# Kernel optimization log

Measured on AMD Instinct MI355X. Metric: run time of the kernel, lower is better.

## Reference

```python
import jax, jax.numpy as jnp
import numpy as np

N = 100000
E = 500000
HID = 256
N_EDGE_TYPES = 5
N_ATOM = 16
N_CHARGE = 7
NUM_RBF = 16
CUTOFF = 5.0
LN_EPS = 1e-5


def _xavier(key, shape):
    fan_in, fan_out = shape[0], shape[1]
    lim = float(np.sqrt(6.0 / (fan_in + fan_out)))
    return jax.random.uniform(key, shape, jnp.float32, -lim, lim)


def setup_inputs() -> dict:
    key = jax.random.key(0)
    ks = jax.random.split(key, 12)
    input_dim = HID * 2 + NUM_RBF + N_ATOM + N_CHARGE  # 551
    h = jax.random.normal(ks[0], (N, HID), jnp.float32)
    x = jax.random.normal(ks[1], (N, 3), jnp.float32)
    spawn_node_idx = jax.random.randint(ks[2], (E,), 0, N)
    existing_node_idx = jax.random.randint(ks[3], (E,), 0, N)
    ins_x = jax.random.normal(ks[4], (E, 3), jnp.float32)
    ins_a = jax.random.randint(ks[5], (E,), 0, N_ATOM)
    ins_c = jax.random.randint(ks[6], (E,), 0, N_CHARGE)
    # MLP params (Xavier weights, zero biases; LayerNorm gamma=1, beta=0)
    W1 = _xavier(ks[7], (input_dim, HID)); b1 = jnp.zeros((HID,), jnp.float32)
    g1 = jnp.ones((HID,), jnp.float32); be1 = jnp.zeros((HID,), jnp.float32)
    W2 = _xavier(ks[8], (HID, HID // 2)); b2 = jnp.zeros((HID // 2,), jnp.float32)
    g2 = jnp.ones((HID // 2,), jnp.float32); be2 = jnp.zeros((HID // 2,), jnp.float32)
    W3 = _xavier(ks[9], (HID // 2, N_EDGE_TYPES)); b3 = jnp.zeros((N_EDGE_TYPES,), jnp.float32)
    # Gaussian RBF parameters: centers on [0, cutoff], shared width from spacing
    rbf_mu = jnp.linspace(0.0, CUTOFF, NUM_RBF).astype(jnp.float32)
    delta = CUTOFF / (NUM_RBF - 1)
    rbf_gamma = jnp.asarray(1.0 / (2.0 * delta * delta), jnp.float32)
    return {"h": h, "x": x, "spawn_node_idx": spawn_node_idx,
            "existing_node_idx": existing_node_idx, "ins_x": ins_x,
            "ins_a": ins_a, "ins_c": ins_c,
            "W1": W1, "b1": b1, "g1": g1, "be1": be1,
            "W2": W2, "b2": b2, "g2": g2, "be2": be2,
            "W3": W3, "b3": b3, "rbf_mu": rbf_mu, "rbf_gamma": rbf_gamma}


def _layer_norm(z, gamma, beta):
    mu = jnp.mean(z, axis=-1, keepdims=True)
    var = jnp.mean((z - mu) ** 2, axis=-1, keepdims=True)
    return (z - mu) * jax.lax.rsqrt(var + LN_EPS) * gamma + beta


def reference(h, x, spawn_node_idx, existing_node_idx, ins_x, ins_a, ins_c,
              W1, b1, g1, be1, W2, b2, g2, be2, W3, b3, rbf_mu, rbf_gamma):
    # gather node pairs  [E, HID] / [E, 3]
    h_spawn = h[spawn_node_idx]
    h_existing = h[existing_node_idx]
    existing_pos = x[existing_node_idx]
    # distance + Gaussian RBF  [E, NUM_RBF]
    d = jnp.maximum(jnp.linalg.norm(ins_x - existing_pos, axis=-1), 1e-6)
    dist_features = jnp.exp(-rbf_gamma * (d[:, None] - rbf_mu) ** 2)
    # one-hot insertion type features
    ins_atom = jax.nn.one_hot(ins_a, N_ATOM, dtype=h.dtype)
    ins_charge = jax.nn.one_hot(ins_c, N_CHARGE, dtype=h.dtype)
    feats = jnp.concatenate([h_spawn, h_existing, dist_features, ins_atom, ins_charge], axis=-1)
    # 3-layer MLP: Linear -> LN -> SiLU -> Linear -> LN -> SiLU -> Linear
    z = jax.nn.silu(_layer_norm(feats @ W1 + b1, g1, be1))
    z = jax.nn.silu(_layer_norm(z @ W2 + b2, g2, be2))
    return z @ W3 + b3  # [E, N_EDGE_TYPES]
```

## Files before the change

### kernel.cpp

```cpp
#include <hip/hip_runtime.h>
#include <stdint.h>

#define NN 100000
#define EE 500000
#define HIDD 256
#define LN_EPS 1e-5f

typedef _Float16 half8 __attribute__((ext_vector_type(8)));
typedef _Float16 half4 __attribute__((ext_vector_type(4)));
typedef __fp16 fp16x2 __attribute__((ext_vector_type(2)));
typedef float f32x4 __attribute__((ext_vector_type(4)));
typedef float f32x2 __attribute__((ext_vector_type(2)));

#define LBAR() asm volatile("s_waitcnt lgkmcnt(0)\n\ts_barrier" ::: "memory")

__device__ __forceinline__ unsigned short f2h(float f) {
  _Float16 h = (_Float16)f;
  union { _Float16 hh; unsigned short us; } u; u.hh = h;
  return u.us;
}

__device__ __forceinline__ unsigned pkrtz(float a, float b) {
  union { fp16x2 h; unsigned u; } c;
  c.h = __builtin_amdgcn_cvt_pkrtz(a, b);
  return c.u;
}

__device__ __forceinline__ float fast_silu(float y) {
  float e = __expf(-y);
  return y * __builtin_amdgcn_rcpf(1.f + e);
}

__device__ __forceinline__ half8 ldg8(const unsigned short* p) {
  return *(const half8*)p;
}

__device__ __forceinline__ int4 cvt_row(const float* s) {
  float4 a0 = *(const float4*)s, a1 = *(const float4*)(s + 4);
  uint4 ua;
  ua.x = pkrtz(a0.x, a0.y); ua.y = pkrtz(a0.z, a0.w);
  ua.z = pkrtz(a1.x, a1.y); ua.w = pkrtz(a1.z, a1.w);
  return *(int4*)&ua;
}


__global__ __launch_bounds__(256) void prep_w(const float* __restrict__ W1,
                                              const float* __restrict__ W2,
                                              const float* __restrict__ W3,
                                              unsigned short* __restrict__ wc,
                                              unsigned short* __restrict__ w1f,
                                              unsigned short* __restrict__ w2sw,
                                              unsigned short* __restrict__ w3sw) {
  int t = blockIdx.x * 256 + threadIdx.x;
  if (t < 131072) {
    int kq = t >> 12, mm = (t >> 3) & 511, j = t & 7;
    int k = kq * 8 + j;
    int row = k + ((mm < 256) ? 0 : 256);
    wc[t] = f2h(W1[row * 256 + (mm & 255)]);
  } else if (t < 147456) {
    int t2 = t - 131072;
    int kq = t2 >> 11, m = (t2 >> 3) & 255, j = t2 & 7;
    int k = 512 + kq * 8 + j;
    w1f[t2] = f2h((k < 551) ? W1[k * 256 + m] : 0.f);
  } else if (t < 180224) {
    int t2 = t - 147456;
    int chunk = t2 >> 13, rem = t2 & 8191;
    int kq = rem >> 10, n = (rem >> 3) & 127, j = rem & 7;
    int k = (chunk << 6) + (kq << 3) + j;
    w2sw[t2] = f2h(W2[k * 128 + n]);
  } else if (t < 182272) {
    int t3 = t - 180224;
    int kq = t3 >> 7, o = (t3 >> 3) & 15, j = t3 & 7;
    int k = (kq << 3) + j;
    w3sw[t3] = f2h((o < 5) ? W3[k * 5 + o] : 0.f);
  }
}

__global__ __launch_bounds__(256) void pgemm(const float* __restrict__ h,
                                             const unsigned short* __restrict__ wc,
                                             unsigned short* __restrict__ Pb) {
  __shared__ short hl[16384];
  const int bid = blockIdx.x;
  const int tile = bid >> 1, ch = bid & 1;
  const int nb = tile * 64;
  const int t = threadIdx.x;
  const int lane = t & 63;
  const int wv = t >> 6;
  const int cl = lane & 15;
  const int q = lane >> 4;
  const int sx = (cl & 7) << 3;

  const int row0 = t >> 3, p0 = t & 7;
  const int row1 = row0 + 32;
  const int n0 = (nb + row0 < NN) ? nb + row0 : NN - 1;
  const int n1 = (nb + row1 < NN) ? nb + row1 : NN - 1;
  const int sw0e = (row0 & 7) << 3;
  const int sw1e = (row1 & 7) << 3;
#pragma unroll
  for (int c = 0; c < 4; ++c) {
    int4 v0 = cvt_row(h + (size_t)n0 * 256 + c * 64 + p0 * 8);
    int4 v1 = cvt_row(h + (size_t)n1 * 256 + c * 64 + p0 * 8);
    *(int4*)&hl[row0 * 256 + ((c * 64 + p0 * 8) ^ sw0e)] = v0;
    *(int4*)&hl[row1 * 256 + ((c * 64 + p0 * 8) ^ sw1e)] = v1;
  }
  LBAR();

  const unsigned short* wcp = wc + q * 4096 + (size_t)(ch * 256 + wv * 64 + cl) * 8;
  f32x4 acc[4][4];
#pragma unroll
  for (int i = 0; i < 4; ++i)
#pragma unroll
    for (int j = 0; j < 4; ++j) acc[i][j] = (f32x4){0.f, 0.f, 0.f, 0.f};

#pragma unroll
  for (int c = 0; c < 4; ++c)
#pragma unroll
    for (int ks = 0; ks < 2; ++ks) {
      half8 bf[4], fX[4];
#pragma unroll
      for (int j = 0; j < 4; ++j)
        bf[j] = *(const half8*)&hl[(j * 16 + cl) * 256 + ((c * 64 + ks * 32 + q * 8) ^ sx)];
#pragma unroll
      for (int i = 0; i < 4; ++i) fX[i] = ldg8(wcp + (c * 2 + ks) * 16384 + i * 128);
#pragma unroll
      for (int i = 0; i < 4; ++i)
#pragma unroll
        for (int j = 0; j < 4; ++j)
          acc[i][j] = __builtin_amdgcn_mfma_f32_16x16x32_f16(fX[i], bf[j], acc[i][j], 0, 0, 0);
    }

#pragma unroll
  for (int i = 0; i < 4; ++i)
#pragma unroll
    for (int j = 0; j < 4; ++j) {
      int n = nb + cl + 16 * j;
      if (n < NN) {
        int mm = ch * 256 + wv * 64 + i * 16 + q * 4;
        uint2 w;
        w.x = pkrtz(acc[i][j][0], acc[i][j][1]);
        w.y = pkrtz(acc[i][j][2], acc[i][j][3]);
        *(uint2*)(Pb + (size_t)n * 512 + mm) = w;
      }
    }
}

struct __align__(16) SMemN {
  short r1[16384];
  short feats[4096];
  float red[512];
  _Float16 b1h[256], g1h[256], be1h[256];
  _Float16 b2h[128], g2h[128], be2h[128];
  float muv[16];
  float b3v[8];
  int spI[64], exI[64];
};

__global__ __launch_bounds__(256, 3)
void edge_head_main(const float* __restrict__ x,
                    const int* __restrict__ spawn, const int* __restrict__ exist,
                    const float* __restrict__ insx, const int* __restrict__ insa,
                    const int* __restrict__ insc,
                    const float* __restrict__ b1, const float* __restrict__ g1,
                    const float* __restrict__ be1,
                    const float* __restrict__ b2, const float* __restrict__ g2,
                    const float* __restrict__ be2,
                    const float* __restrict__ b3, const float* __restrict__ mu,
                    const float* __restrict__ gammaP,
                    const unsigned short* __restrict__ w1f,
                    const unsigned short* __restrict__ w2sw,
                    const unsigned short* __restrict__ w3swg,
                    const unsigned short* __restrict__ Pb,
                    float* __restrict__ out) {
  __shared__ SMemN sm;
  const int t = threadIdx.x;
  const int base = blockIdx.x * 64;
  const int lane = t & 63;
  const int wv = t >> 6;
  const int cl = lane & 15;
  const int q = lane >> 4;
  const int sx = (cl & 7) << 3;

  sm.b1h[t] = (_Float16)b1[t]; sm.g1h[t] = (_Float16)g1[t]; sm.be1h[t] = (_Float16)be1[t];
  if (t < 128) { sm.b2h[t] = (_Float16)b2[t]; sm.g2h[t] = (_Float16)g2[t]; sm.be2h[t] = (_Float16)be2[t]; }
  if (t < 16) sm.muv[t] = mu[t];
  if (t < 8) sm.b3v[t] = (t < 5) ? b3[t] : 0.f;
  if (t < 64) {
    int e = base + t; int ec = e < EE ? e : EE - 1;
    sm.spI[t] = spawn[ec]; sm.exI[t] = exist[ec];
  }
  const float gma = gammaP[0];

  LBAR();

  const unsigned short* pb1[4];
  const unsigned short* pb2[4];
#pragma unroll
  for (int j = 0; j < 4; ++j) {
    int n = cl + 16 * j;
    pb1[j] = Pb + (size_t)sm.spI[n] * 512 + wv * 64 + q * 4;
    pb2[j] = Pb + (size_t)sm.exI[n] * 512 + 256 + wv * 64 + q * 4;
  }
  half4 p1v[4][4], p2v[4][4];
#pragma unroll
  for (int i = 0; i < 4; ++i)
#pragma unroll
    for (int j = 0; j < 4; ++j) p1v[i][j] = *(const half4*)(pb1[j] + i * 16);
#pragma unroll
  for (int i = 0; i < 4; ++i)
#pragma unroll
    for (int j = 0; j < 4; ++j) p2v[i][j] = *(const half4*)(pb2[j] + i * 16);

  if (t < 64) {
    int e = base + t; int ec = e < EE ? e : EE - 1;
    float ix0 = insx[ec * 3], ix1 = insx[ec * 3 + 1], ix2 = insx[ec * 3 + 2];
    int nd = sm.exI[t];
    float dx = ix0 - x[nd * 3], dy = ix1 - x[nd * 3 + 1], dz = ix2 - x[nd * 3 + 2];
    float d = fmaxf(sqrtf(dx * dx + dy * dy + dz * dz), 1e-6f);
    int k1 = 16 + insa[ec], k2 = 32 + insc[ec];
    short* rp = &sm.feats[t * 64];
    const int sw = t & 7;
    float rb[16];
#pragma unroll
    for (int k = 0; k < 16; ++k) { float dd = d - sm.muv[k]; rb[k] = __expf(-gma * dd * dd); }
    uint4 ua, ub;
    ua.x = pkrtz(rb[0], rb[1]);  ua.y = pkrtz(rb[2], rb[3]);
    ua.z = pkrtz(rb[4], rb[5]);  ua.w = pkrtz(rb[6], rb[7]);
    ub.x = pkrtz(rb[8], rb[9]);  ub.y = pkrtz(rb[10], rb[11]);
    ub.z = pkrtz(rb[12], rb[13]); ub.w = pkrtz(rb[14], rb[15]);
    *(int4*)&rp[(0 ^ sw) * 8] = *(int4*)&ua;
    *(int4*)&rp[(1 ^ sw) * 8] = *(int4*)&ub;
    const int4 z4 = {0, 0, 0, 0};
#pragma unroll
    for (int g = 2; g < 8; ++g) *(int4*)&rp[(g ^ sw) * 8] = z4;
    rp[((k1 >> 3) ^ sw) * 8 + (k1 & 7)] = (short)0x3C00;
    rp[((k2 >> 3) ^ sw) * 8 + (k2 & 7)] = (short)0x3C00;
  }

  LBAR();

  f32x4 acc[4][4];
#pragma unroll
  for (int i = 0; i < 4; ++i)
#pragma unroll
    for (int j = 0; j < 4; ++j) {
      f32x4 a;
      a[0] = (float)p1v[i][j][0] + (float)p2v[i][j][0];
      a[1] = (float)p1v[i][j][1] + (float)p2v[i][j][1];
      a[2] = (float)p1v[i][j][2] + (float)p2v[i][j][2];
      a[3] = (float)p1v[i][j][3] + (float)p2v[i][j][3];
      acc[i][j] = a;
    }
  {
    const unsigned short* w1fp = w1f + q * 2048 + wv * 512 + cl * 8;
#pragma unroll
    for (int ks = 0; ks < 2; ++ks) {
      half8 bf[4], fX[4];
#pragma unroll
      for (int j = 0; j < 4; ++j)
        bf[j] = *(const half8*)&sm.feats[(j * 16 + cl) * 64 + ((ks * 32 + q * 8) ^ sx)];
#pragma unroll
      for (int i = 0; i < 4; ++i) fX[i] = ldg8(w1fp + ks * 8192 + i * 128);
#pragma unroll
      for (int i = 0; i < 4; ++i)
#pragma unroll
        for (int j = 0; j < 4; ++j)
          acc[i][j] = __builtin_amdgcn_mfma_f32_16x16x32_f16(fX[i], bf[j], acc[i][j], 0, 0, 0);
    }
  }

  f32x2 bb1[4][2];
#pragma unroll
  for (int i = 0; i < 4; ++i) {
    half4 b4 = *(const half4*)&sm.b1h[wv * 64 + i * 16 + q * 4];
    bb1[i][0] = (f32x2){(float)b4[0], (float)b4[1]};
    bb1[i][1] = (f32x2){(float)b4[2], (float)b4[3]};
  }
  float S1arr[4], Q1arr[4];
#pragma unroll
  for (int j = 0; j < 4; ++j) {
    f32x2 S2 = (f32x2){0.f, 0.f}, Q2 = (f32x2){0.f, 0.f};
#pragma unroll
    for (int i = 0; i < 4; ++i) {
      f32x2 v0 = (f32x2){acc[i][j][0], acc[i][j][1]} + bb1[i][0];
      f32x2 v1 = (f32x2){acc[i][j][2], acc[i][j][3]} + bb1[i][1];
      acc[i][j][0] = v0[0]; acc[i][j][1] = v0[1];
      acc[i][j][2] = v1[0]; acc[i][j][3] = v1[1];
      S2 += v0 + v1;
      Q2 += v0 * v0;
      Q2 += v1 * v1;
    }
    float S = S2[0] + S2[1], Q = Q2[0] + Q2[1];
    S += __shfl_xor(S, 16); S += __shfl_xor(S, 32);
    Q += __shfl_xor(Q, 16); Q += __shfl_xor(Q, 32);
    S1arr[j] = S; Q1arr[j] = Q;
  }
  if (q == 0) {
#pragma unroll
    for (int j = 0; j < 4; ++j) {
      sm.red[wv * 64 + j * 16 + cl] = S1arr[j];
      sm.red[256 + wv * 64 + j * 16 + cl] = Q1arr[j];
    }
  }
  LBAR();
  f32x2 rs1[4], mr1[4];
#pragma unroll
  for (int j = 0; j < 4; ++j) {
    int m = j * 16 + cl;
    float S = sm.red[m] + sm.red[64 + m] + sm.red[128 + m] + sm.red[192 + m];
    float Q = sm.red[256 + m] + sm.red[320 + m] + sm.red[384 + m] + sm.red[448 + m];
    float mn = S * (1.f / 256.f);
    float rs = rsqrtf(Q * (1.f / 256.f) - mn * mn + LN_EPS);
    rs1[j] = (f32x2){rs, rs};
    mr1[j] = (f32x2){-mn * rs, -mn * rs};
  }
#pragma unroll
  for (int i = 0; i < 4; ++i) {
    half4 g4 = *(const half4*)&sm.g1h[wv * 64 + i * 16 + q * 4];
    half4 e4 = *(const half4*)&sm.be1h[wv * 64 + i * 16 + q * 4];
    f32x2 gg0 = (f32x2){(float)g4[0], (float)g4[1]}, gg1 = (f32x2){(float)g4[2], (float)g4[3]};
    f32x2 ee0 = (f32x2){(float)e4[0], (float)e4[1]}, ee1 = (f32x2){(float)e4[2], (float)e4[3]};
#pragma unroll
    for (int j = 0; j < 4; ++j) {
      f32x2 v0 = (f32x2){acc[i][j][0], acc[i][j][1]};
      f32x2 v1 = (f32x2){acc[i][j][2], acc[i][j][3]};
      f32x2 t0 = v0 * rs1[j] + mr1[j];
      f32x2 t1 = v1 * rs1[j] + mr1[j];
      f32x2 y0 = t0 * gg0 + ee0;
      f32x2 y1 = t1 * gg1 + ee1;
      float s0 = fast_silu(y0[0]), s1 = fast_silu(y0[1]);
      float s2 = fast_silu(y1[0]), s3 = fast_silu(y1[1]);
      uint2 w; w.x = pkrtz(s0, s1); w.y = pkrtz(s2, s3);
      int m = j * 16 + cl;
      int k0 = wv * 64 + i * 16 + q * 4;
      *(uint2*)&sm.r1[m * 256 + (k0 ^ ((m & 7) << 3))] = w;
    }
  }
  LBAR();

  half8 af3[4];
#pragma unroll
  for (int ks = 0; ks < 4; ++ks)
    af3[ks] = ldg8(w3swg + (ks * 4 + q) * 128 + cl * 8);

  const unsigned short* w2p = w2sw + q * 1024 + wv * 256 + cl * 8;
  f32x4 acc2[2][4];
#pragma unroll
  for (int i = 0; i < 2; ++i)
#pragma unroll
    for (int j = 0; j < 4; ++j) acc2[i][j] = (f32x4){0.f, 0.f, 0.f, 0.f};
#pragma unroll
  for (int c2 = 0; c2 < 4; ++c2) {
#pragma unroll
    for (int ks = 0; ks < 2; ++ks) {
      half8 a0 = ldg8(w2p + c2 * 8192 + ks * 4096);
      half8 a1 = ldg8(w2p + c2 * 8192 + ks * 4096 + 128);
      half8 bf[4];
#pragma unroll
      for (int j = 0; j < 4; ++j)
        bf[j] = *(const half8*)&sm.r1[(j * 16 + cl) * 256 + ((c2 * 64 + ks * 32 + q * 8) ^ sx)];
#pragma unroll
      for (int j = 0; j < 4; ++j) {
        acc2[0][j] = __builtin_amdgcn_mfma_f32_16x16x32_f16(a0, bf[j], acc2[0][j], 0, 0, 0);
        acc2[1][j] = __builtin_amdgcn_mfma_f32_16x16x32_f16(a1, bf[j], acc2[1][j], 0, 0, 0);
      }
    }
  }

  f32x2 bb2[2][2];
#pragma unroll
  for (int i = 0; i < 2; ++i) {
    half4 b4 = *(const half4*)&sm.b2h[wv * 32 + i * 16 + q * 4];
    bb2[i][0] = (f32x2){(float)b4[0], (float)b4[1]};
    bb2[i][1] = (f32x2){(float)b4[2], (float)b4[3]};
  }
  float S2arr[4], Q2arr[4];
#pragma unroll
  for (int j = 0; j < 4; ++j) {
    f32x2 S2 = (f32x2){0.f, 0.f}, Q2 = (f32x2){0.f, 0.f};
#pragma unroll
    for (int i = 0; i < 2; ++i) {
      f32x2 v0 = (f32x2){acc2[i][j][0], acc2[i][j][1]} + bb2[i][0];
      f32x2 v1 = (f32x2){acc2[i][j][2], acc2[i][j][3]} + bb2[i][1];
      acc2[i][j][0] = v0[0]; acc2[i][j][1] = v0[1];
      acc2[i][j][2] = v1[0]; acc2[i][j][3] = v1[1];
      S2 += v0 + v1;
      Q2 += v0 * v0;
      Q2 += v1 * v1;
    }
    float S = S2[0] + S2[1], Q = Q2[0] + Q2[1];
    S += __shfl_xor(S, 16); S += __shfl_xor(S, 32);
    Q += __shfl_xor(Q, 16); Q += __shfl_xor(Q, 32);
    S2arr[j] = S; Q2arr[j] = Q;
  }
  if (q == 0) {
#pragma unroll
    for (int j = 0; j < 4; ++j) {
      sm.red[wv * 64 + j * 16 + cl] = S2arr[j];
      sm.red[256 + wv * 64 + j * 16 + cl] = Q2arr[j];
    }
  }
  LBAR();
  f32x2 rs2[4], mr2[4];
#pragma unroll
  for (int j = 0; j < 4; ++j) {
    int m = j * 16 + cl;
    float S = sm.red[m] + sm.red[64 + m] + sm.red[128 + m] + sm.red[192 + m];
    float Q = sm.red[256 + m] + sm.red[320 + m] + sm.red[384 + m] + sm.red[448 + m];
    float mn = S * (1.f / 128.f);
    float rs = rsqrtf(Q * (1.f / 128.f) - mn * mn + LN_EPS);
    rs2[j] = (f32x2){rs, rs};
    mr2[j] = (f32x2){-mn * rs, -mn * rs};
  }
#pragma unroll
  for (int i = 0; i < 2; ++i) {
    half4 g4 = *(const half4*)&sm.g2h[wv * 32 + i * 16 + q * 4];
    half4 e4 = *(const half4*)&sm.be2h[wv * 32 + i * 16 + q * 4];
    f32x2 gg0 = (f32x2){(float)g4[0], (float)g4[1]}, gg1 = (f32x2){(float)g4[2], (float)g4[3]};
    f32x2 ee0 = (f32x2){(float)e4[0], (float)e4[1]}, ee1 = (f32x2){(float)e4[2], (float)e4[3]};
#pragma unroll
    for (int j = 0; j < 4; ++j) {
      f32x2 v0 = (f32x2){acc2[i][j][0], acc2[i][j][1]};
      f32x2 v1 = (f32x2){acc2[i][j][2], acc2[i][j][3]};
      f32x2 t0 = v0 * rs2[j] + mr2[j];
      f32x2 t1 = v1 * rs2[j] + mr2[j];
      f32x2 y0 = t0 * gg0 + ee0;
      f32x2 y1 = t1 * gg1 + ee1;
      float s0 = fast_silu(y0[0]), s1 = fast_silu(y0[1]);
      float s2 = fast_silu(y1[0]), s3 = fast_silu(y1[1]);
      uint2 w; w.x = pkrtz(s0, s1); w.y = pkrtz(s2, s3);
      int m = j * 16 + cl;
      int k0 = wv * 32 + i * 16 + q * 4;
      *(uint2*)&sm.r1[m * 128 + (k0 ^ ((m & 7) << 3))] = w;
    }
  }
  LBAR();

  f32x4 a3 = (f32x4){0.f, 0.f, 0.f, 0.f};
  const int m3 = wv * 16 + cl;
  const int sx3 = (m3 & 7) << 3;
#pragma unroll
  for (int ks = 0; ks < 4; ++ks) {
    half8 bfv = *(const half8*)&sm.r1[m3 * 128 + ((ks * 32 + q * 8) ^ sx3)];
    a3 = __builtin_amdgcn_mfma_f32_16x16x32_f16(af3[ks], bfv, a3, 0, 0, 0);
  }
#pragma unroll
  for (int r = 0; r < 4; ++r) {
    int o = q * 4 + r;
    if (o < 5) sm.red[m3 * 5 + o] = a3[r] + sm.b3v[o];
  }
  LBAR();
  if (t < 80) {
    size_t g = (size_t)base * 5 + (size_t)t * 4;
    if (g + 4 <= (size_t)EE * 5) {
      *(float4*)(out + g) = *(const float4*)&sm.red[t * 4];
    } else {
#pragma unroll
      for (int u = 0; u < 4; ++u)
        if (g + u < (size_t)EE * 5) out[g + u] = sm.red[t * 4 + u];
    }
  }
}


__global__ __launch_bounds__(256) void prep_fb(const float* __restrict__ W1,
                                               const float* __restrict__ W2,
                                               const float* __restrict__ W3,
                                               unsigned short* __restrict__ w1sw,
                                               unsigned short* __restrict__ w2sw,
                                               unsigned short* __restrict__ w3sw) {
  int t = blockIdx.x * 256 + threadIdx.x;
  if (t < 147456) {
    int chunk = t >> 14, rem = t & 16383;
    int kq = rem >> 11, n = (rem >> 3) & 255, j = rem & 7;
    int k = (chunk << 6) + (kq << 3) + j;
    w1sw[t] = f2h((k < 551) ? W1[k * 256 + n] : 0.f);
  } else if (t < 180224) {
    int t2 = t - 147456;
    int chunk = t2 >> 13, rem = t2 & 8191;
    int kq = rem >> 10, n = (rem >> 3) & 127, j = rem & 7;
    int k = (chunk << 6) + (kq << 3) + j;
    w2sw[t2] = f2h(W2[k * 128 + n]);
  } else if (t < 182272) {
    int t3 = t - 180224;
    int kq = t3 >> 7, o = (t3 >> 3) & 15, j = t3 & 7;
    int k = (kq << 3) + j;
    w3sw[t3] = f2h((o < 5) ? W3[k * 5 + o] : 0.f);
  }
}

struct __align__(16) SMemF {
  short r1[16384];
  short feats[4096];
  float red[512];
  _Float16 b1h[256], g1h[256], be1h[256];
  _Float16 b2h[128], g2h[128], be2h[128];
  float muv[16];
  float b3v[8];
  int spI[64], exI[64];
};

__global__ __launch_bounds__(256, 3)
void edge_head_fb(const float* __restrict__ h, const float* __restrict__ x,
                  const int* __restrict__ spawn, const int* __restrict__ exist,
                  const float* __restrict__ insx, const int* __restrict__ insa,
                  const int* __restrict__ insc,
                  const float* __restrict__ b1, const float* __restrict__ g1,
                  const float* __restrict__ be1,
                  const float* __restrict__ b2, const float* __restrict__ g2,
                  const float* __restrict__ be2,
                  const float* __restrict__ b3, const float* __restrict__ mu,
                  const float* __restrict__ gammaP,
                  const unsigned short* __restrict__ w1sw,
                  const unsigned short* __restrict__ w2sw,
                  const unsigned short* __restrict__ w3swg,
                  float* __restrict__ out) {
  __shared__ SMemF sm;
  const int t = threadIdx.x;
  const int base = blockIdx.x * 64;
  const int lane = t & 63;
  const int wv = t >> 6;
  const int cl = lane & 15;
  const int q = lane >> 4;
  const int sx = (cl & 7) << 3;

  sm.b1h[t] = (_Float16)b1[t]; sm.g1h[t] = (_Float16)g1[t]; sm.be1h[t] = (_Float16)be1[t];
  if (t < 128) { sm.b2h[t] = (_Float16)b2[t]; sm.g2h[t] = (_Float16)g2[t]; sm.be2h[t] = (_Float16)be2[t]; }
  if (t < 16) sm.muv[t] = mu[t];
  if (t < 8) sm.b3v[t] = (t < 5) ? b3[t] : 0.f;
  if (t < 64) {
    int e = base + t; int ec = e < EE ? e : EE - 1;
    sm.spI[t] = spawn[ec]; sm.exI[t] = exist[ec];
  }
  const float gma = gammaP[0];
  LBAR();

  float dreg = 0.f;
  int k1 = 16, k2 = 32;
  if (t < 64) {
    int e = base + t; int ec = e < EE ? e : EE - 1;
    float ix0 = insx[ec * 3], ix1 = insx[ec * 3 + 1], ix2 = insx[ec * 3 + 2];
    int nd = sm.exI[t];
    float dx = ix0 - x[nd * 3], dy = ix1 - x[nd * 3 + 1], dz = ix2 - x[nd * 3 + 2];
    dreg = fmaxf(sqrtf(dx * dx + dy * dy + dz * dz), 1e-6f);
    k1 = 16 + insa[ec]; k2 = 32 + insc[ec];
  }

  const int row0 = t >> 3, p0 = t & 7;
  const int row1 = row0 + 32;
  const int sw0 = ((p0 ^ (row0 & 7)) << 3);
  const int sw1 = ((p0 ^ (row1 & 7)) << 3);

  const float* bSp0 = h + (size_t)sm.spI[row0] * HIDD + p0 * 8;
  const float* bSp1 = h + (size_t)sm.spI[row1] * HIDD + p0 * 8;
  const float* bEx0 = h + (size_t)sm.exI[row0] * HIDD + p0 * 8;
  const float* bEx1 = h + (size_t)sm.exI[row1] * HIDD + p0 * 8;

  int4 pS0, pS1, pS2, pS3;
#define GLOAD2F(ph) do {                                                \
    const float* b0_ = ((ph) < 2) ? bSp0 : bEx0;                        \
    const float* b1_ = ((ph) < 2) ? bSp1 : bEx1;                        \
    const int ce_ = ((ph) & 1) * 128;                                   \
    pS0 = cvt_row(b0_ + ce_);                                           \
    pS1 = cvt_row(b1_ + ce_);                                           \
    pS2 = cvt_row(b0_ + ce_ + 64);                                      \
    pS3 = cvt_row(b1_ + ce_ + 64);                                      \
  } while (0)

  GLOAD2F(0);
  *(int4*)&sm.r1[row0 * 64 + sw0] = pS0;
  *(int4*)&sm.r1[row1 * 64 + sw1] = pS1;
  *(int4*)&sm.r1[4096 + row0 * 64 + sw0] = pS2;
  *(int4*)&sm.r1[4096 + row1 * 64 + sw1] = pS3;
  GLOAD2F(1);

  const unsigned short* w1p = w1sw + q * 2048 + wv * 512 + cl * 8;

  if (t < 64) {
    short* rp = &sm.feats[t * 64];
    const int sw = t & 7;
    float rb[16];
#pragma unroll
    for (int k = 0; k < 16; ++k) { float dd = dreg - sm.muv[k]; rb[k] = __expf(-gma * dd * dd); }
    uint4 ua, ub;
    ua.x = pkrtz(rb[0], rb[1]);  ua.y = pkrtz(rb[2], rb[3]);
    ua.z = pkrtz(rb[4], rb[5]);  ua.w = pkrtz(rb[6], rb[7]);
    ub.x = pkrtz(rb[8], rb[9]);  ub.y = pkrtz(rb[10], rb[11]);
    ub.z = pkrtz(rb[12], rb[13]); ub.w = pkrtz(rb[14], rb[15]);
    *(int4*)&rp[(0 ^ sw) * 8] = *(int4*)&ua;
    *(int4*)&rp[(1 ^ sw) * 8] = *(int4*)&ub;
    const int4 z4 = {0, 0, 0, 0};
#pragma unroll
    for (int g = 2; g < 8; ++g) *(int4*)&rp[(g ^ sw) * 8] = z4;
    rp[((k1 >> 3) ^ sw) * 8 + (k1 & 7)] = (short)0x3C00;
    rp[((k2 >> 3) ^ sw) * 8 + (k2 & 7)] = (short)0x3C00;
  }
  LBAR();

  f32x4 acc[4][4];
#pragma unroll
  for (int i = 0; i < 4; ++i)
#pragma unroll
    for (int j = 0; j < 4; ++j) acc[i][j] = (f32x4){0.f, 0.f, 0.f, 0.f};

#pragma unroll
  for (int p = 0; p < 4; ++p) {
    if (p < 3) {
      const int nb = ((p + 1) & 1) * 8192;
      *(int4*)&sm.r1[nb + row0 * 64 + sw0] = pS0;
      *(int4*)&sm.r1[nb + row1 * 64 + sw1] = pS1;
      *(int4*)&sm.r1[nb + 4096 + row0 * 64 + sw0] = pS2;
      *(int4*)&sm.r1[nb + 4096 + row1 * 64 + sw1] = pS3;
      if (p < 2) GLOAD2F(p + 2);
    }
    const int cb = (p & 1) * 8192;
#pragma unroll
    for (int ch = 0; ch < 2; ++ch) {
      const unsigned short* wp = w1p + (2 * p + ch) * 16384;
#pragma unroll
      for (int ks = 0; ks < 2; ++ks) {
        half8 bf[4], fX[4];
#pragma unroll
        for (int j = 0; j < 4; ++j)
          bf[j] = *(const half8*)&sm.r1[cb + ch * 4096 + (j * 16 + cl) * 64 + ((ks * 32 + q * 8) ^ sx)];
#pragma unroll
        for (int i = 0; i < 4; ++i) fX[i] = ldg8(wp + ks * 8192 + i * 128);
#pragma unroll
        for (int i = 0; i < 4; ++i)
#pragma unroll
          for (int j = 0; j < 4; ++j)
            acc[i][j] = __builtin_amdgcn_mfma_f32_16x16x32_f16(fX[i], bf[j], acc[i][j], 0, 0, 0);
      }
    }
    if (p < 3) LBAR();
  }
#undef GLOAD2F

  {
    const unsigned short* wp = w1p + 8 * 16384;
#pragma unroll
    for (int ks = 0; ks < 2; ++ks) {
      half8 bf[4], fX[4];
#pragma unroll
      for (int j = 0; j < 4; ++j)
        bf[j] = *(const half8*)&sm.feats[(j * 16 + cl) * 64 + ((ks * 32 + q * 8) ^ sx)];
#pragma unroll
      for (int i = 0; i < 4; ++i) fX[i] = ldg8(wp + ks * 8192 + i * 128);
#pragma unroll
      for (int i = 0; i < 4; ++i)
#pragma unroll
        for (int j = 0; j < 4; ++j)
          acc[i][j] = __builtin_amdgcn_mfma_f32_16x16x32_f16(fX[i], bf[j], acc[i][j], 0, 0, 0);
    }
  }

  f32x2 bb1[4][2];
#pragma unroll
  for (int i = 0; i < 4; ++i) {
    half4 b4 = *(const half4*)&sm.b1h[wv * 64 + i * 16 + q * 4];
    bb1[i][0] = (f32x2){(float)b4[0], (float)b4[1]};
    bb1[i][1] = (f32x2){(float)b4[2], (float)b4[3]};
  }
  float S1arr[4], Q1arr[4];
#pragma unroll
  for (int j = 0; j < 4; ++j) {
    f32x2 S2 = (f32x2){0.f, 0.f}, Q2 = (f32x2){0.f, 0.f};
#pragma unroll
    for (int i = 0; i < 4; ++i) {
      f32x2 v0 = (f32x2){acc[i][j][0], acc[i][j][1]} + bb1[i][0];
      f32x2 v1 = (f32x2){acc[i][j][2], acc[i][j][3]} + bb1[i][1];
      acc[i][j][0] = v0[0]; acc[i][j][1] = v0[1];
      acc[i][j][2] = v1[0]; acc[i][j][3] = v1[1];
      S2 += v0 + v1; Q2 += v0 * v0; Q2 += v1 * v1;
    }
    float S = S2[0] + S2[1], Q = Q2[0] + Q2[1];
    S += __shfl_xor(S, 16); S += __shfl_xor(S, 32);
    Q += __shfl_xor(Q, 16); Q += __shfl_xor(Q, 32);
    S1arr[j] = S; Q1arr[j] = Q;
  }
  if (q == 0) {
#pragma unroll
    for (int j = 0; j < 4; ++j) {
      sm.red[wv * 64 + j * 16 + cl] = S1arr[j];
      sm.red[256 + wv * 64 + j * 16 + cl] = Q1arr[j];
    }
  }
  LBAR();
  f32x2 rs1[4], mr1[4];
#pragma unroll
  for (int j = 0; j < 4; ++j) {
    int m = j * 16 + cl;
    float S = sm.red[m] + sm.red[64 + m] + sm.red[128 + m] + sm.red[192 + m];
    float Q = sm.red[256 + m] + sm.red[320 + m] + sm.red[384 + m] + sm.red[448 + m];
    float mn = S * (1.f / 256.f);
    float rs = rsqrtf(Q * (1.f / 256.f) - mn * mn + LN_EPS);
    rs1[j] = (f32x2){rs, rs};
    mr1[j] = (f32x2){-mn * rs, -mn * rs};
  }
#pragma unroll
  for (int i = 0; i < 4; ++i) {
    half4 g4 = *(const half4*)&sm.g1h[wv * 64 + i * 16 + q * 4];
    half4 e4 = *(const half4*)&sm.be1h[wv * 64 + i * 16 + q * 4];
    f32x2 gg0 = (f32x2){(float)g4[0], (float)g4[1]}, gg1 = (f32x2){(float)g4[2], (float)g4[3]};
    f32x2 ee0 = (f32x2){(float)e4[0], (float)e4[1]}, ee1 = (f32x2){(float)e4[2], (float)e4[3]};
#pragma unroll
    for (int j = 0; j < 4; ++j) {
      f32x2 v0 = (f32x2){acc[i][j][0], acc[i][j][1]};
      f32x2 v1 = (f32x2){acc[i][j][2], acc[i][j][3]};
      f32x2 t0 = v0 * rs1[j] + mr1[j];
      f32x2 t1 = v1 * rs1[j] + mr1[j];
      f32x2 y0 = t0 * gg0 + ee0;
      f32x2 y1 = t1 * gg1 + ee1;
      float s0 = fast_silu(y0[0]), s1 = fast_silu(y0[1]);
      float s2 = fast_silu(y1[0]), s3 = fast_silu(y1[1]);
      uint2 w; w.x = pkrtz(s0, s1); w.y = pkrtz(s2, s3);
      int m = j * 16 + cl;
      int k0 = wv * 64 + i * 16 + q * 4;
      *(uint2*)&sm.r1[m * 256 + (k0 ^ ((m & 7) << 3))] = w;
    }
  }
  LBAR();

  half8 af3[4];
#pragma unroll
  for (int ks = 0; ks < 4; ++ks)
    af3[ks] = ldg8(w3swg + (ks * 4 + q) * 128 + cl * 8);

  const unsigned short* w2p = w2sw + q * 1024 + wv * 256 + cl * 8;
  f32x4 acc2[2][4];
#pragma unroll
  for (int i = 0; i < 2; ++i)
#pragma unroll
    for (int j = 0; j < 4; ++j) acc2[i][j] = (f32x4){0.f, 0.f, 0.f, 0.f};
#pragma unroll
  for (int c2 = 0; c2 < 4; ++c2) {
#pragma unroll
    for (int ks = 0; ks < 2; ++ks) {
      half8 a0 = ldg8(w2p + c2 * 8192 + ks * 4096);
      half8 a1 = ldg8(w2p + c2 * 8192 + ks * 4096 + 128);
      half8 bf[4];
#pragma unroll
      for (int j = 0; j < 4; ++j)
        bf[j] = *(const half8*)&sm.r1[(j * 16 + cl) * 256 + ((c2 * 64 + ks * 32 + q * 8) ^ sx)];
#pragma unroll
      for (int j = 0; j < 4; ++j) {
        acc2[0][j] = __builtin_amdgcn_mfma_f32_16x16x32_f16(a0, bf[j], acc2[0][j], 0, 0, 0);
        acc2[1][j] = __builtin_amdgcn_mfma_f32_16x16x32_f16(a1, bf[j], acc2[1][j], 0, 0, 0);
      }
    }
  }

  f32x2 bb2[2][2];
#pragma unroll
  for (int i = 0; i < 2; ++i) {
    half4 b4 = *(const half4*)&sm.b2h[wv * 32 + i * 16 + q * 4];
    bb2[i][0] = (f32x2){(float)b4[0], (float)b4[1]};
    bb2[i][1] = (f32x2){(float)b4[2], (float)b4[3]};
  }
  float S2arr[4], Q2arr[4];
#pragma unroll
  for (int j = 0; j < 4; ++j) {
    f32x2 S2 = (f32x2){0.f, 0.f}, Q2 = (f32x2){0.f, 0.f};
#pragma unroll
    for (int i = 0; i < 2; ++i) {
      f32x2 v0 = (f32x2){acc2[i][j][0], acc2[i][j][1]} + bb2[i][0];
      f32x2 v1 = (f32x2){acc2[i][j][2], acc2[i][j][3]} + bb2[i][1];
      acc2[i][j][0] = v0[0]; acc2[i][j][1] = v0[1];
      acc2[i][j][2] = v1[0]; acc2[i][j][3] = v1[1];
      S2 += v0 + v1; Q2 += v0 * v0; Q2 += v1 * v1;
    }
    float S = S2[0] + S2[1], Q = Q2[0] + Q2[1];
    S += __shfl_xor(S, 16); S += __shfl_xor(S, 32);
    Q += __shfl_xor(Q, 16); Q += __shfl_xor(Q, 32);
    S2arr[j] = S; Q2arr[j] = Q;
  }
  if (q == 0) {
#pragma unroll
    for (int j = 0; j < 4; ++j) {
      sm.red[wv * 64 + j * 16 + cl] = S2arr[j];
      sm.red[256 + wv * 64 + j * 16 + cl] = Q2arr[j];
    }
  }
  LBAR();
  f32x2 rs2[4], mr2[4];
#pragma unroll
  for (int j = 0; j < 4; ++j) {
    int m = j * 16 + cl;
    float S = sm.red[m] + sm.red[64 + m] + sm.red[128 + m] + sm.red[192 + m];
    float Q = sm.red[256 + m] + sm.red[320 + m] + sm.red[384 + m] + sm.red[448 + m];
    float mn = S * (1.f / 128.f);
    float rs = rsqrtf(Q * (1.f / 128.f) - mn * mn + LN_EPS);
    rs2[j] = (f32x2){rs, rs};
    mr2[j] = (f32x2){-mn * rs, -mn * rs};
  }
#pragma unroll
  for (int i = 0; i < 2; ++i) {
    half4 g4 = *(const half4*)&sm.g2h[wv * 32 + i * 16 + q * 4];
    half4 e4 = *(const half4*)&sm.be2h[wv * 32 + i * 16 + q * 4];
    f32x2 gg0 = (f32x2){(float)g4[0], (float)g4[1]}, gg1 = (f32x2){(float)g4[2], (float)g4[3]};
    f32x2 ee0 = (f32x2){(float)e4[0], (float)e4[1]}, ee1 = (f32x2){(float)e4[2], (float)e4[3]};
#pragma unroll
    for (int j = 0; j < 4; ++j) {
      f32x2 v0 = (f32x2){acc2[i][j][0], acc2[i][j][1]};
      f32x2 v1 = (f32x2){acc2[i][j][2], acc2[i][j][3]};
      f32x2 t0 = v0 * rs2[j] + mr2[j];
      f32x2 t1 = v1 * rs2[j] + mr2[j];
      f32x2 y0 = t0 * gg0 + ee0;
      f32x2 y1 = t1 * gg1 + ee1;
      float s0 = fast_silu(y0[0]), s1 = fast_silu(y0[1]);
      float s2 = fast_silu(y1[0]), s3 = fast_silu(y1[1]);
      uint2 w; w.x = pkrtz(s0, s1); w.y = pkrtz(s2, s3);
      int m = j * 16 + cl;
      int k0 = wv * 32 + i * 16 + q * 4;
      *(uint2*)&sm.r1[m * 128 + (k0 ^ ((m & 7) << 3))] = w;
    }
  }
  LBAR();

  f32x4 a3 = (f32x4){0.f, 0.f, 0.f, 0.f};
  const int m3 = wv * 16 + cl;
  const int sx3 = (m3 & 7) << 3;
#pragma unroll
  for (int ks = 0; ks < 4; ++ks) {
    half8 bfv = *(const half8*)&sm.r1[m3 * 128 + ((ks * 32 + q * 8) ^ sx3)];
    a3 = __builtin_amdgcn_mfma_f32_16x16x32_f16(af3[ks], bfv, a3, 0, 0, 0);
  }
#pragma unroll
  for (int r = 0; r < 4; ++r) {
    int o = q * 4 + r;
    if (o < 5) sm.red[m3 * 5 + o] = a3[r] + sm.b3v[o];
  }
  LBAR();
  if (t < 80) {
    size_t g = (size_t)base * 5 + (size_t)t * 4;
    if (g + 4 <= (size_t)EE * 5) {
      *(float4*)(out + g) = *(const float4*)&sm.red[t * 4];
    } else {
#pragma unroll
      for (int u = 0; u < 4; ++u)
        if (g + u < (size_t)EE * 5) out[g + u] = sm.red[t * 4 + u];
    }
  }
}

extern "C" void kernel_launch(void* const* d_in, const int* in_sizes, int n_in,
                              void* d_out, int out_size, void* d_ws, size_t ws_size,
                              hipStream_t stream) {
  const float* h    = (const float*)d_in[0];
  const float* x    = (const float*)d_in[1];
  const int* spawn  = (const int*)d_in[2];
  const int* exist  = (const int*)d_in[3];
  const float* insx = (const float*)d_in[4];
  const int* insa   = (const int*)d_in[5];
  const int* insc   = (const int*)d_in[6];
  const float* W1   = (const float*)d_in[7];
  const float* b1   = (const float*)d_in[8];
  const float* g1   = (const float*)d_in[9];
  const float* be1  = (const float*)d_in[10];
  const float* W2   = (const float*)d_in[11];
  const float* b2   = (const float*)d_in[12];
  const float* g2   = (const float*)d_in[13];
  const float* be2  = (const float*)d_in[14];
  const float* W3   = (const float*)d_in[15];
  const float* b3   = (const float*)d_in[16];
  const float* mu   = (const float*)d_in[17];
  const float* gma  = (const float*)d_in[18];

  const size_t needP = 364544ull + (size_t)NN * 512 * 2;
  if (ws_size >= needP) {
    unsigned short* wc   = (unsigned short*)d_ws;
    unsigned short* w1f  = wc + 131072;
    unsigned short* w2sw = w1f + 16384;
    unsigned short* w3sw = w2sw + 32768;
    unsigned short* Pb   = w3sw + 2048;
    prep_w<<<712, 256, 0, stream>>>(W1, W2, W3, wc, w1f, w2sw, w3sw);
    pgemm<<<3126, 256, 0, stream>>>(h, wc, Pb);
    edge_head_main<<<7813, 256, 0, stream>>>(x, spawn, exist, insx, insa, insc,
                                             b1, g1, be1, b2, g2, be2, b3, mu, gma,
                                             w1f, w2sw, w3sw, Pb, (float*)d_out);
  } else {
    unsigned short* w1sw = (unsigned short*)d_ws;
    unsigned short* w2sw = w1sw + 147456;
    unsigned short* w3sw = w2sw + 32768;
    prep_fb<<<712, 256, 0, stream>>>(W1, W2, W3, w1sw, w2sw, w3sw);
    edge_head_fb<<<7813, 256, 0, stream>>>(h, x, spawn, exist, insx, insa, insc,
                                           b1, g1, be1, b2, g2, be2, b3, mu, gma,
                                           w1sw, w2sw, w3sw, (float*)d_out);
  }
}
```

Measured before the change: 427.4 us.

## Merge pgemm column halves, fold bias into projection, raise edge kernel occupancy

New measurement: 434.8 us. Within noise of the previous version (+1.7%).

```diff
diff --git a/kernel.cpp b/kernel.cpp
--- a/kernel.cpp
+++ b/kernel.cpp
@@ -77,12 +77,11 @@
 }
 
 __global__ __launch_bounds__(256) void pgemm(const float* __restrict__ h,
+                                             const float* __restrict__ b1,
                                              const unsigned short* __restrict__ wc,
                                              unsigned short* __restrict__ Pb) {
   __shared__ short hl[16384];
-  const int bid = blockIdx.x;
-  const int tile = bid >> 1, ch = bid & 1;
-  const int nb = tile * 64;
+  const int nb = blockIdx.x * 64;
   const int t = threadIdx.x;
   const int lane = t & 63;
   const int wv = t >> 6;
@@ -105,63 +104,71 @@
   }
   LBAR();
 
-  const unsigned short* wcp = wc + q * 4096 + (size_t)(ch * 256 + wv * 64 + cl) * 8;
-  f32x4 acc[4][4];
-#pragma unroll
-  for (int i = 0; i < 4; ++i)
-#pragma unroll
-    for (int j = 0; j < 4; ++j) acc[i][j] = (f32x4){0.f, 0.f, 0.f, 0.f};
-
-#pragma unroll
-  for (int c = 0; c < 4; ++c)
-#pragma unroll
-    for (int ks = 0; ks < 2; ++ks) {
-      half8 bf[4], fX[4];
-#pragma unroll
-      for (int j = 0; j < 4; ++j)
-        bf[j] = *(const half8*)&hl[(j * 16 + cl) * 256 + ((c * 64 + ks * 32 + q * 8) ^ sx)];
-#pragma unroll
-      for (int i = 0; i < 4; ++i) fX[i] = ldg8(wcp + (c * 2 + ks) * 16384 + i * 128);
+#pragma unroll
+  for (int ch = 0; ch < 2; ++ch) {
+    const unsigned short* wcp = wc + q * 4096 + (size_t)(ch * 256 + wv * 64 + cl) * 8;
+    f32x4 acc[4][4];
+    if (ch == 0) {
+#pragma unroll
+      for (int i = 0; i < 4; ++i) {
+        float4 bv = *(const float4*)(b1 + wv * 64 + i * 16 + q * 4);
+#pragma unroll
+        for (int j = 0; j < 4; ++j) acc[i][j] = (f32x4){bv.x, bv.y, bv.z, bv.w};
+      }
+    } else {
 #pragma unroll
       for (int i = 0; i < 4; ++i)
 #pragma unroll
+        for (int j = 0; j < 4; ++j) acc[i][j] = (f32x4){0.f, 0.f, 0.f, 0.f};
+    }
+#pragma unroll
+    for (int c = 0; c < 4; ++c)
+#pragma unroll
+      for (int ks = 0; ks < 2; ++ks) {
+        half8 bf[4], fX[4];
+#pragma unroll
         for (int j = 0; j < 4; ++j)
-          acc[i][j] = __builtin_amdgcn_mfma_f32_16x16x32_f16(fX[i], bf[j], acc[i][j], 0, 0, 0);
-    }
-
-#pragma unroll
-  for (int i = 0; i < 4; ++i)
-#pragma unroll
-    for (int j = 0; j < 4; ++j) {
-      int n = nb + cl + 16 * j;
-      if (n < NN) {
-        int mm = ch * 256 + wv * 64 + i * 16 + q * 4;
-        uint2 w;
-        w.x = pkrtz(acc[i][j][0], acc[i][j][1]);
-        w.y = pkrtz(acc[i][j][2], acc[i][j][3]);
-        *(uint2*)(Pb + (size_t)n * 512 + mm) = w;
+          bf[j] = *(const half8*)&hl[(j * 16 + cl) * 256 + ((c * 64 + ks * 32 + q * 8) ^ sx)];
+#pragma unroll
+        for (int i = 0; i < 4; ++i) fX[i] = ldg8(wcp + (c * 2 + ks) * 16384 + i * 128);
+#pragma unroll
+        for (int i = 0; i < 4; ++i)
+#pragma unroll
+          for (int j = 0; j < 4; ++j)
+            acc[i][j] = __builtin_amdgcn_mfma_f32_16x16x32_f16(fX[i], bf[j], acc[i][j], 0, 0, 0);
       }
-    }
+#pragma unroll
+    for (int i = 0; i < 4; ++i)
+#pragma unroll
+      for (int j = 0; j < 4; ++j) {
+        int n = nb + cl + 16 * j;
+        if (n < NN) {
+          int mm = ch * 256 + wv * 64 + i * 16 + q * 4;
+          uint2 w;
+          w.x = pkrtz(acc[i][j][0], acc[i][j][1]);
+          w.y = pkrtz(acc[i][j][2], acc[i][j][3]);
+          *(uint2*)(Pb + (size_t)n * 512 + mm) = w;
+        }
+      }
+  }
 }
 
 struct __align__(16) SMemN {
   short r1[16384];
-  short feats[4096];
   float red[512];
-  _Float16 b1h[256], g1h[256], be1h[256];
+  _Float16 g1h[256], be1h[256];
   _Float16 b2h[128], g2h[128], be2h[128];
   float muv[16];
   float b3v[8];
   int spI[64], exI[64];
 };
 
-__global__ __launch_bounds__(256, 3)
+__global__ __launch_bounds__(256, 4)
 void edge_head_main(const float* __restrict__ x,
                     const int* __restrict__ spawn, const int* __restrict__ exist,
                     const float* __restrict__ insx, const int* __restrict__ insa,
                     const int* __restrict__ insc,
-                    const float* __restrict__ b1, const float* __restrict__ g1,
-                    const float* __restrict__ be1,
+                    const float* __restrict__ g1, const float* __restrict__ be1,
                     const float* __restrict__ b2, const float* __restrict__ g2,
                     const float* __restrict__ be2,
                     const float* __restrict__ b3, const float* __restrict__ mu,
@@ -180,7 +187,7 @@
   const int q = lane >> 4;
   const int sx = (cl & 7) << 3;
 
-  sm.b1h[t] = (_Float16)b1[t]; sm.g1h[t] = (_Float16)g1[t]; sm.be1h[t] = (_Float16)be1[t];
+  sm.g1h[t] = (_Float16)g1[t]; sm.be1h[t] = (_Float16)be1[t];
   if (t < 128) { sm.b2h[t] = (_Float16)b2[t]; sm.g2h[t] = (_Float16)g2[t]; sm.be2h[t] = (_Float16)be2[t]; }
   if (t < 16) sm.muv[t] = mu[t];
   if (t < 8) sm.b3v[t] = (t < 5) ? b3[t] : 0.f;
@@ -200,15 +207,15 @@
     pb1[j] = Pb + (size_t)sm.spI[n] * 512 + wv * 64 + q * 4;
     pb2[j] = Pb + (size_t)sm.exI[n] * 512 + 256 + wv * 64 + q * 4;
   }
-  half4 p1v[4][4], p2v[4][4];
-#pragma unroll
-  for (int i = 0; i < 4; ++i)
-#pragma unroll
-    for (int j = 0; j < 4; ++j) p1v[i][j] = *(const half4*)(pb1[j] + i * 16);
-#pragma unroll
-  for (int i = 0; i < 4; ++i)
-#pragma unroll
-    for (int j = 0; j < 4; ++j) p2v[i][j] = *(const half4*)(pb2[j] + i * 16);
+  half4 p1a[2][4], p2a[2][4];
+#pragma unroll
+  for (int i2 = 0; i2 < 2; ++i2)
+#pragma unroll
+    for (int j = 0; j < 4; ++j) p1a[i2][j] = *(const half4*)(pb1[j] + i2 * 16);
+#pragma unroll
+  for (int i2 = 0; i2 < 2; ++i2)
+#pragma unroll
+    for (int j = 0; j < 4; ++j) p2a[i2][j] = *(const half4*)(pb2[j] + i2 * 16);
 
   if (t < 64) {
     int e = base + t; int ec = e < EE ? e : EE - 1;
@@ -217,7 +224,7 @@
     float dx = ix0 - x[nd * 3], dy = ix1 - x[nd * 3 + 1], dz = ix2 - x[nd * 3 + 2];
     float d = fmaxf(sqrtf(dx * dx + dy * dy + dz * dz), 1e-6f);
     int k1 = 16 + insa[ec], k2 = 32 + insc[ec];
-    short* rp = &sm.feats[t * 64];
+    short* rp = &sm.r1[t * 64];
     const int sw = t & 7;
     float rb[16];
 #pragma unroll
@@ -236,19 +243,40 @@
     rp[((k2 >> 3) ^ sw) * 8 + (k2 & 7)] = (short)0x3C00;
   }
 
+  half4 p1b[2][4], p2b[2][4];
+#pragma unroll
+  for (int i2 = 0; i2 < 2; ++i2)
+#pragma unroll
+    for (int j = 0; j < 4; ++j) p1b[i2][j] = *(const half4*)(pb1[j] + (2 + i2) * 16);
+#pragma unroll
+  for (int i2 = 0; i2 < 2; ++i2)
+#pragma unroll
+    for (int j = 0; j < 4; ++j) p2b[i2][j] = *(const half4*)(pb2[j] + (2 + i2) * 16);
+
   LBAR();
 
   f32x4 acc[4][4];
 #pragma unroll
-  for (int i = 0; i < 4; ++i)
+  for (int i2 = 0; i2 < 2; ++i2)
 #pragma unroll
     for (int j = 0; j < 4; ++j) {
       f32x4 a;
-      a[0] = (float)p1v[i][j][0] + (float)p2v[i][j][0];
-      a[1] = (float)p1v[i][j][1] + (float)p2v[i][j][1];
-      a[2] = (float)p1v[i][j][2] + (float)p2v[i][j][2];
-      a[3] = (float)p1v[i][j][3] + (float)p2v[i][j][3];
-      acc[i][j] = a;
+      a[0] = (float)p1a[i2][j][0] + (float)p2a[i2][j][0];
+      a[1] = (float)p1a[i2][j][1] + (float)p2a[i2][j][1];
+      a[2] = (float)p1a[i2][j][2] + (float)p2a[i2][j][2];
+      a[3] = (float)p1a[i2][j][3] + (float)p2a[i2][j][3];
+      acc[i2][j] = a;
+    }
+#pragma unroll
+  for (int i2 = 0; i2 < 2; ++i2)
+#pragma unroll
+    for (int j = 0; j < 4; ++j) {
+      f32x4 a;
+      a[0] = (float)p1b[i2][j][0] + (float)p2b[i2][j][0];
+      a[1] = (float)p1b[i2][j][1] + (float)p2b[i2][j][1];
+      a[2] = (float)p1b[i2][j][2] + (float)p2b[i2][j][2];
+      a[3] = (float)p1b[i2][j][3] + (float)p2b[i2][j][3];
+      acc[2 + i2][j] = a;
     }
   {
     const unsigned short* w1fp = w1f + q * 2048 + wv * 512 + cl * 8;
@@ -257,7 +285,7 @@
       half8 bf[4], fX[4];
 #pragma unroll
       for (int j = 0; j < 4; ++j)
-        bf[j] = *(const half8*)&sm.feats[(j * 16 + cl) * 64 + ((ks * 32 + q * 8) ^ sx)];
+        bf[j] = *(const half8*)&sm.r1[(j * 16 + cl) * 64 + ((ks * 32 + q * 8) ^ sx)];
 #pragma unroll
       for (int i = 0; i < 4; ++i) fX[i] = ldg8(w1fp + ks * 8192 + i * 128);
 #pragma unroll
@@ -268,23 +296,14 @@
     }
   }
 
-  f32x2 bb1[4][2];
-#pragma unroll
-  for (int i = 0; i < 4; ++i) {
-    half4 b4 = *(const half4*)&sm.b1h[wv * 64 + i * 16 + q * 4];
-    bb1[i][0] = (f32x2){(float)b4[0], (float)b4[1]};
-    bb1[i][1] = (f32x2){(float)b4[2], (float)b4[3]};
-  }
   float S1arr[4], Q1arr[4];
 #pragma unroll
   for (int j = 0; j < 4; ++j) {
     f32x2 S2 = (f32x2){0.f, 0.f}, Q2 = (f32x2){0.f, 0.f};
 #pragma unroll
     for (int i = 0; i < 4; ++i) {
-      f32x2 v0 = (f32x2){acc[i][j][0], acc[i][j][1]} + bb1[i][0];
-      f32x2 v1 = (f32x2){acc[i][j][2], acc[i][j][3]} + bb1[i][1];
-      acc[i][j][0] = v0[0]; acc[i][j][1] = v0[1];
-      acc[i][j][2] = v1[0]; acc[i][j][3] = v1[1];
+      f32x2 v0 = (f32x2){acc[i][j][0], acc[i][j][1]};
+      f32x2 v1 = (f32x2){acc[i][j][2], acc[i][j][3]};
       S2 += v0 + v1;
       Q2 += v0 * v0;
       Q2 += v1 * v1;
@@ -460,7 +479,6 @@
     }
   }
 }
-
 
 __global__ __launch_bounds__(256) void prep_fb(const float* __restrict__ W1,
                                                const float* __restrict__ W2,
@@ -873,9 +891,9 @@
     unsigned short* w3sw = w2sw + 32768;
     unsigned short* Pb   = w3sw + 2048;
     prep_w<<<712, 256, 0, stream>>>(W1, W2, W3, wc, w1f, w2sw, w3sw);
-    pgemm<<<3126, 256, 0, stream>>>(h, wc, Pb);
+    pgemm<<<1563, 256, 0, stream>>>(h, b1, wc, Pb);
     edge_head_main<<<7813, 256, 0, stream>>>(x, spawn, exist, insx, insa, insc,
-                                             b1, g1, be1, b2, g2, be2, b3, mu, gma,
+                                             g1, be1, b2, g2, be2, b3, mu, gma,
                                              w1f, w2sw, w3sw, Pb, (float*)d_out);
   } else {
     unsigned short* w1sw = (unsigned short*)d_ws;
```
